# Optimization experiments

Hardware: AMD Instinct MI355X
Metric: run time of the kernel (lower is better)

Reference implementation:

```python
import jax, jax.numpy as jnp
import numpy as np

ALPHA = 2.0   # ATan surrogate alpha (spikingjelly default)
VTH = 0.5     # v_threshold
NUM_HEADS = 8

@jax.custom_vjp
def atan_spike(x):
    return (x >= 0.0).astype(x.dtype)

def _atan_fwd(x):
    return atan_spike(x), x

def _atan_bwd(x, g):
    return (g * (ALPHA / 2.0) / (1.0 + (jnp.pi / 2.0 * ALPHA * x) ** 2),)

atan_spike.defvjp(_atan_fwd, _atan_bwd)

def lif(x, w):
    # ParametricLIFNode, step_mode='m', decay_input=True, v_reset=0 (hard reset), detach_reset
    sg = jax.nn.sigmoid(w)
    def step(v, xt):
        v = v + (xt - v) * sg
        s = atan_spike(v - VTH)
        v = v * (1.0 - jax.lax.stop_gradient(s))  # hard reset to 0, detached
        return v, s
    _, spikes = jax.lax.scan(step, jnp.zeros_like(x[0]), x)
    return spikes

def bn_eT(x, gamma, beta, eps=1e-5):
    # x: [T, B, C, N]; per-(T,C) channel stats over (B, N)  == BatchNorm1d on [B, T*C, N] (train mode)
    T, B, C, N = x.shape
    mean = x.mean(axis=(1, 3), keepdims=True)
    var = jnp.mean((x - mean) ** 2, axis=(1, 3), keepdims=True)
    g = gamma.reshape(T, 1, C, 1)
    b = beta.reshape(T, 1, C, 1)
    return (x - mean) * jax.lax.rsqrt(var + eps) * g + b

def setup_inputs() -> dict:
    key = jax.random.key(0)
    ks = jax.random.split(key, 6)
    T, B, N, C = 16, 8, 196, 512
    return {
        "x": jax.random.normal(ks[0], (T, B, N, C), dtype=jnp.float32),
        "qkv_w": jax.random.normal(ks[1], (3 * C, C), dtype=jnp.float32) * 0.02,
        "qkv_b": jax.random.normal(ks[2], (3 * C,), dtype=jnp.float32) * 0.02,
        "bn1_g": jnp.ones((T * 3 * C,), dtype=jnp.float32),
        "bn1_b": jnp.zeros((T * 3 * C,), dtype=jnp.float32),
        "proj_w": jax.random.normal(ks[3], (C, C), dtype=jnp.float32) * 0.02,
        "proj_b": jax.random.normal(ks[4], (C,), dtype=jnp.float32) * 0.02,
        "bn2_g": jnp.ones((T * C,), dtype=jnp.float32),
        "bn2_b": jnp.zeros((T * C,), dtype=jnp.float32),
        "w_in": jnp.zeros((), dtype=jnp.float32),
        "w_q": jnp.zeros((), dtype=jnp.float32),
        "w_k": jnp.zeros((), dtype=jnp.float32),
        "w_v": jnp.zeros((), dtype=jnp.float32),
        "w_proj": jnp.zeros((), dtype=jnp.float32),
    }

def reference(x, qkv_w, qkv_b, bn1_g, bn1_b, proj_w, proj_b, bn2_g, bn2_b,
              w_in, w_q, w_k, w_v, w_proj):
    T, B, N, C = x.shape
    H = NUM_HEADS
    hd = C // H
    scale = hd ** -0.5

    x = lif(x, w_in)                                            # [T,B,N,C] spikes
    qkv = jnp.einsum('tbnc,oc->tbno', x, qkv_w) + qkv_b         # [T,B,N,3C]
    qkv = bn_eT(jnp.swapaxes(qkv, -2, -1), bn1_g, bn1_b)        # [T,B,3C,N]
    qkv = jnp.swapaxes(qkv, -2, -1).reshape(T, B, N, 3, H, hd)
    qkv = jnp.transpose(qkv, (3, 0, 1, 4, 2, 5))                # [3,T,B,H,N,hd]

    q_sk = lif(qkv[0], w_q)
    k_sk = lif(qkv[1], w_k)
    v_sk = lif(qkv[2], w_v)

    kv = jnp.einsum('tbhnd,tbhne->tbhde', k_sk, v_sk)           # k^T @ v : [T,B,H,hd,hd]
    out = jnp.einsum('tbhnd,tbhde->tbhne', q_sk, kv) * scale    # [T,B,H,N,hd]
    out = jnp.transpose(out, (0, 1, 3, 2, 4)).reshape(T, B, N, C)

    out = lif(out, w_proj)
    out = jnp.einsum('tbnc,oc->tbno', out, proj_w) + proj_b     # [T,B,N,C]
    out = bn_eT(jnp.swapaxes(out, -2, -1), bn2_g, bn2_b)        # [T,B,C,N]
    return jnp.swapaxes(out, -2, -1)                            # [T,B,N,C]
```

## Files before the change

kernel.cpp:

```cpp
#include <hip/hip_runtime.h>


#define TT 16
#define BB 8
#define NNQ 196
#define CC 512
#define HH 8
#define HD 64
#define O3 1536
#define BN (BB*NNQ)
#define PT (BN*CC)
#define WTOT ((O3+CC)*CC)
#define NRG 14

static constexpr float VTH = 0.5f;
typedef __attribute__((ext_vector_type(8))) short short8;
typedef __attribute__((ext_vector_type(4))) float f32x4;
typedef unsigned short u16;

__device__ __forceinline__ float sigm(float w){ return 1.f/(1.f+expf(-w)); }

__device__ __forceinline__ float lif_step(float x, float& v, float sg){
  float d  = __fsub_rn(x, v);
  float dd = __fmul_rn(d, sg);
  v = __fadd_rn(v, dd);
  float sp = (v >= VTH) ? 1.f : 0.f;
  v = __fmul_rn(v, __fsub_rn(1.f, sp));
  return sp;
}

__device__ __forceinline__ u16 bf16_rn(float x){
  unsigned u = __float_as_uint(x);
  unsigned r = u + 0x7FFF + ((u>>16)&1);
  return (u16)(r>>16);
}
__device__ __forceinline__ float bf16_to_f(u16 h){
  return __uint_as_float(((unsigned)h)<<16);
}

__global__ void k_wsplit(const float* __restrict__ qkv_w, const float* __restrict__ proj_w,
                         u16* __restrict__ whi, u16* __restrict__ wmid, u16* __restrict__ wlo){
  int i = blockIdx.x*256 + threadIdx.x;
  float w = (i < O3*CC) ? qkv_w[i] : proj_w[i - O3*CC];
  u16 h = bf16_rn(w);          float r1 = w - bf16_to_f(h);
  u16 m = bf16_rn(r1);         float r2 = r1 - bf16_to_f(m);
  u16 l = bf16_rn(r2);
  whi[i]=h; wmid[i]=m; wlo[i]=l;
}

__global__ void k_lif_x(const float* __restrict__ x, const float* __restrict__ w,
                        float* __restrict__ vin, u16* __restrict__ s0, int t0, int tc){
  int g = blockIdx.x*256 + threadIdx.x;
  float sg = sigm(w[0]);
  float v = (t0==0) ? 0.f : vin[g];
  for (int tt=0; tt<tc; ++tt){
    float sp = lif_step(x[(size_t)(t0+tt)*PT + g], v, sg);
    s0[(size_t)tt*PT + g] = (sp!=0.f) ? 0x3F80 : 0;
  }
  vin[g] = v;
}

template<int ON>
__global__ __launch_bounds__(256)
void k_gemm_mfma(const u16* __restrict__ A, const u16* __restrict__ Wh,
                 const u16* __restrict__ Wm, const u16* __restrict__ Wl,
                 const float* __restrict__ bias, float* __restrict__ Cm, int M){
  __shared__ __align__(16) u16 Al[128][64];
  __shared__ __align__(16) u16 Bh[128][64];
  __shared__ __align__(16) u16 Bm[128][64];
  __shared__ __align__(16) u16 Bl[128][64];
  int tid = threadIdx.x;
  int w = tid>>6, lane = tid&63;
  int m0 = blockIdx.x*128, o0 = blockIdx.y*128;
  int wm = (w&1)*64, wn = (w>>1)*64;
  int r16 = lane&15, kg = lane>>4;
  f32x4 acc[4][4] = {};
  for (int k0=0;k0<512;k0+=64){
    #pragma unroll
    for (int i=0;i<4;++i){
      int u = tid*4 + i;
      int row = u>>3, slot = u&7;
      int sl = slot ^ (row&7);
      int gr = m0+row; if (gr>=M) gr=M-1;
      *(float4*)&Al[row][sl*8] = *(const float4*)&A [(size_t)gr*512      + k0 + slot*8];
      *(float4*)&Bh[row][sl*8] = *(const float4*)&Wh[(size_t)(o0+row)*512 + k0 + slot*8];
      *(float4*)&Bm[row][sl*8] = *(const float4*)&Wm[(size_t)(o0+row)*512 + k0 + slot*8];
      *(float4*)&Bl[row][sl*8] = *(const float4*)&Wl[(size_t)(o0+row)*512 + k0 + slot*8];
    }
    __syncthreads();
    #pragma unroll
    for (int s=0;s<2;++s){
      short8 af[4], bh[4], bm[4], bl[4];
      #pragma unroll
      for (int mt=0;mt<4;++mt){
        int r = wm + mt*16 + r16;
        af[mt] = *(const short8*)&Al[r][((s*4+kg)^(r&7))*8];
      }
      #pragma unroll
      for (int nt=0;nt<4;++nt){
        int r = wn + nt*16 + r16;
        int sl = ((s*4+kg)^(r&7))*8;
        bh[nt] = *(const short8*)&Bh[r][sl];
        bm[nt] = *(const short8*)&Bm[r][sl];
        bl[nt] = *(const short8*)&Bl[r][sl];
      }
      #pragma unroll
      for (int mt=0;mt<4;++mt)
        #pragma unroll
        for (int nt=0;nt<4;++nt){
          acc[mt][nt] = __builtin_amdgcn_mfma_f32_16x16x32_bf16(af[mt], bh[nt], acc[mt][nt],0,0,0);
          acc[mt][nt] = __builtin_amdgcn_mfma_f32_16x16x32_bf16(af[mt], bm[nt], acc[mt][nt],0,0,0);
          acc[mt][nt] = __builtin_amdgcn_mfma_f32_16x16x32_bf16(af[mt], bl[nt], acc[mt][nt],0,0,0);
        }
    }
    __syncthreads();
  }
  #pragma unroll
  for (int mt=0; mt<4; ++mt)
    #pragma unroll
    for (int nt=0; nt<4; ++nt){
      int o = o0 + wn + nt*16 + r16;
      float bs = bias[o];
      #pragma unroll
      for (int i=0;i<4;++i){
        int m = m0 + wm + mt*16 + kg*4 + i;
        if (m < M) Cm[(size_t)m*ON + o] = acc[mt][nt][i] + bs;
      }
    }
}

template<int O>
__global__ void k_stat_part(const float* __restrict__ X, double* __restrict__ psum,
                            double* __restrict__ psq){
  int o = blockIdx.x*64 + threadIdx.x;
  int tt = blockIdx.y;
  int rg = blockIdx.z;
  const float* Xb = X + (size_t)tt*BN*O;
  int r0 = rg*112;
  double sum=0.0, sq=0.0;
  for (int i=r0+threadIdx.y; i<r0+112; i+=4){
    double v = (double)Xb[(size_t)i*O + o];
    sum += v; sq += v*v;
  }
  __shared__ double ssum[4][64], ssq[4][64];
  ssum[threadIdx.y][threadIdx.x]=sum;
  ssq [threadIdx.y][threadIdx.x]=sq;
  __syncthreads();
  if (threadIdx.y==0){
    double s = ssum[0][threadIdx.x]+ssum[1][threadIdx.x]+ssum[2][threadIdx.x]+ssum[3][threadIdx.x];
    double q = ssq [0][threadIdx.x]+ssq [1][threadIdx.x]+ssq [2][threadIdx.x]+ssq [3][threadIdx.x];
    size_t idx = ((size_t)tt*O + o)*NRG + rg;
    psum[idx]=s; psq[idx]=q;
  }
}

template<int O, int TCN>
__global__ void k_stat_reduce(const double* __restrict__ psum, const double* __restrict__ psq,
                              float* __restrict__ mean, float* __restrict__ rstd){
  int i = blockIdx.x*256 + threadIdx.x;
  if (i >= TCN*O) return;
  double s=0.0, q=0.0;
  #pragma unroll
  for (int g=0; g<NRG; ++g){ s += psum[(size_t)i*NRG+g]; q += psq[(size_t)i*NRG+g]; }
  double m = s*(1.0/BN);
  double var = q*(1.0/BN) - m*m;
  mean[i]=(float)m;
  rstd[i]=(float)(1.0/sqrt(var+1e-5));
}

__global__ void k_lif_qkv(const float* __restrict__ qkv, const float* __restrict__ mean,
                          const float* __restrict__ rstd, const float* __restrict__ g1,
                          const float* __restrict__ b1,
                          const float* __restrict__ wq, const float* __restrict__ wk,
                          const float* __restrict__ wv,
                          float* __restrict__ vq, float* __restrict__ vk, float* __restrict__ vv,
                          u16* __restrict__ qs, u16* __restrict__ ks,
                          u16* __restrict__ vs, int t0, int tc){
  int g = blockIdx.x*256 + threadIdx.x;
  int j = blockIdx.y;
  int d = g & 63;
  int n = (g>>6) % NNQ;
  int h = (g/(NNQ*64)) & 7;
  int b = g/(NNQ*64*8);
  int o = j*CC + h*HD + d;
  const float* w = (j==0)? wq : (j==1)? wk : wv;
  float* st  = (j==0)? vq : (j==1)? vk : vv;
  u16* out = (j==0)? qs : (j==1)? ks : vs;
  float sg = sigm(w[0]);
  float v = (t0==0) ? 0.f : st[g];
  size_t row = (size_t)(b*NNQ + n)*O3 + o;
  for (int tt=0; tt<tc; ++tt){
    float xv = qkv[(size_t)tt*BN*O3 + row];
    int so = tt*O3 + o;
    int go = (t0+tt)*O3 + o;
    float xn = __fadd_rn(__fmul_rn(__fmul_rn(__fsub_rn(xv, mean[so]), rstd[so]),
                                   g1[go]), b1[go]);
    float sp = lif_step(xn, v, sg);
    out[(size_t)tt*PT + g] = (sp!=0.f) ? 0x3F80 : 0;
  }
  st[g] = v;
}

__global__ __launch_bounds__(256)
void k_kvqv_mfma(const u16* __restrict__ ks, const u16* __restrict__ vs,
                 const u16* __restrict__ qs, float* __restrict__ attn){
  __shared__ __align__(16) u16 Kb[224][64];
  __shared__ __align__(16) u16 Vb[224][64];
  __shared__ __align__(16) u16 kvb[64][64];
  int blk = blockIdx.x;
  size_t base = (size_t)blk * (NNQ*HD);
  int tid = threadIdx.x, w = tid>>6, lane = tid&63;
  int r16 = lane&15, kg = lane>>4;
  for (int u=tid; u<224*8; u+=256){
    int row=u>>3, slot=u&7;
    float4 z = {0.f,0.f,0.f,0.f};
    float4 kd = z, vd = z;
    if (row < NNQ){
      kd = *(const float4*)&ks[base + (size_t)row*64 + slot*8];
      vd = *(const float4*)&vs[base + (size_t)row*64 + slot*8];
    }
    *(float4*)&Kb[row][slot*8] = kd;
    *(float4*)&Vb[row][slot*8] = vd;
  }
  __syncthreads();
  f32x4 acc[4] = {};
  int d0 = w*16;
  for (int n0=0;n0<224;n0+=32){
    short8 af;
    #pragma unroll
    for (int jj=0;jj<8;++jj) af[jj] = (short)Kb[n0+kg*8+jj][d0 + r16];
    #pragma unroll
    for (int nt=0;nt<4;++nt){
      short8 bf;
      #pragma unroll
      for (int jj=0;jj<8;++jj) bf[jj] = (short)Vb[n0+kg*8+jj][nt*16 + r16];
      acc[nt] = __builtin_amdgcn_mfma_f32_16x16x32_bf16(af, bf, acc[nt],0,0,0);
    }
  }
  #pragma unroll
  for (int nt=0;nt<4;++nt)
    #pragma unroll
    for (int i=0;i<4;++i)
      kvb[d0 + kg*4 + i][nt*16 + r16] = (u16)(__float_as_uint(acc[nt][i])>>16);
  __syncthreads();
  for (int u=tid; u<224*8; u+=256){
    int row=u>>3, slot=u&7;
    int sl = slot ^ (row&7);
    float4 qd = {0.f,0.f,0.f,0.f};
    if (row < NNQ) qd = *(const float4*)&qs[base + (size_t)row*64 + slot*8];
    *(float4*)&Kb[row][sl*8] = qd;
  }
  __syncthreads();
  short8 bkv[2][4];
  #pragma unroll
  for (int s=0;s<2;++s)
    #pragma unroll
    for (int nt=0;nt<4;++nt){
      short8 bf;
      #pragma unroll
      for (int jj=0;jj<8;++jj) bf[jj] = (short)kvb[s*32 + kg*8 + jj][nt*16 + r16];
      bkv[s][nt] = bf;
    }
  for (int mt=w; mt<13; mt+=4){
    f32x4 a2[4] = {};
    short8 qa[2];
    #pragma unroll
    for (int s=0;s<2;++s){
      int r = mt*16 + r16;
      qa[s] = *(const short8*)&Kb[r][(((s*4+kg)^(r&7)))*8];
    }
    #pragma unroll
    for (int s=0;s<2;++s)
      #pragma unroll
      for (int nt=0;nt<4;++nt)
        a2[nt] = __builtin_amdgcn_mfma_f32_16x16x32_bf16(qa[s], bkv[s][nt], a2[nt],0,0,0);
    #pragma unroll
    for (int nt=0;nt<4;++nt){
      int e = nt*16 + r16;
      #pragma unroll
      for (int i=0;i<4;++i){
        int n = mt*16 + kg*4 + i;
        if (n < NNQ) attn[base + (size_t)n*64 + e] = a2[nt][i]*0.125f;
      }
    }
  }
}

__global__ void k_lif_attn(const float* __restrict__ ain, const float* __restrict__ w,
                           float* __restrict__ vo, u16* __restrict__ sp, int t0, int tc){
  int g = blockIdx.x*256 + threadIdx.x;
  int e = g & 63;
  int n = (g>>6) % NNQ;
  int h = (g/(NNQ*64)) & 7;
  int b = g/(NNQ*64*8);
  size_t dst = (size_t)(b*NNQ + n)*CC + h*HD + e;
  float sg = sigm(w[0]);
  float v = (t0==0) ? 0.f : vo[g];
  for (int tt=0; tt<tc; ++tt){
    float s = lif_step(ain[(size_t)tt*PT + g], v, sg);
    sp[(size_t)tt*PT + dst] = (s!=0.f) ? 0x3F80 : 0;
  }
  vo[g] = v;
}

__global__ void k_bn2_apply(const float* __restrict__ X, const float* __restrict__ mean,
                            const float* __restrict__ rstd, const float* __restrict__ g2,
                            const float* __restrict__ b2, float* __restrict__ Y, int t0){
  size_t idx = ((size_t)blockIdx.x*256 + threadIdx.x)*4;
  int tt = (int)(idx / PT);
  size_t off = idx - (size_t)tt*PT;
  int c = (int)(off & (CC-1));
  float4 xv = *(const float4*)&X[idx];
  float4 mv = *(const float4*)&mean[tt*CC + c];
  float4 rv = *(const float4*)&rstd[tt*CC + c];
  float4 gv = *(const float4*)&g2[(t0+tt)*CC + c];
  float4 bv = *(const float4*)&b2[(t0+tt)*CC + c];
  float4 yv;
  yv.x = __fadd_rn(__fmul_rn(__fmul_rn(__fsub_rn(xv.x, mv.x), rv.x), gv.x), bv.x);
  yv.y = __fadd_rn(__fmul_rn(__fmul_rn(__fsub_rn(xv.y, mv.y), rv.y), gv.y), bv.y);
  yv.z = __fadd_rn(__fmul_rn(__fmul_rn(__fsub_rn(xv.z, mv.z), rv.z), gv.z), bv.z);
  yv.w = __fadd_rn(__fmul_rn(__fmul_rn(__fsub_rn(xv.w, mv.w), rv.w), gv.w), bv.w);
  *(float4*)&Y[(size_t)(t0+tt)*PT + off] = yv;
}

extern "C" void kernel_launch(void* const* d_in, const int* in_sizes, int n_in,
                              void* d_out, int out_size, void* d_ws, size_t ws_size,
                              hipStream_t stream){
  const float* x      = (const float*)d_in[0];
  const float* qkv_w  = (const float*)d_in[1];
  const float* qkv_b  = (const float*)d_in[2];
  const float* bn1_g  = (const float*)d_in[3];
  const float* bn1_b  = (const float*)d_in[4];
  const float* proj_w = (const float*)d_in[5];
  const float* proj_b = (const float*)d_in[6];
  const float* bn2_g  = (const float*)d_in[7];
  const float* bn2_b  = (const float*)d_in[8];
  const float* w_in   = (const float*)d_in[9];
  const float* w_q    = (const float*)d_in[10];
  const float* w_k    = (const float*)d_in[11];
  const float* w_v    = (const float*)d_in[12];
  const float* w_proj = (const float*)d_in[13];
  float* outp = (float*)d_out;

  auto need = [](int tc)->size_t{
    return 4ull*5*PT + 8ull*tc*O3 + 8ull*tc*CC
         + 16ull*tc*O3*NRG + 16ull*tc*CC*NRG
         + 6ull*WTOT
         + 10ull*tc*PT
         + 4ull*tc*BN*O3;
  };
  int TC = 16;
  while (TC > 1 && need(TC) > ws_size) TC >>= 1;

  char* p = (char*)d_ws;
  float* vin = (float*)p; p += 4ull*PT;
  float* vq  = (float*)p; p += 4ull*PT;
  float* vk  = (float*)p; p += 4ull*PT;
  float* vv  = (float*)p; p += 4ull*PT;
  float* vo  = (float*)p; p += 4ull*PT;
  float* mean1 = (float*)p; p += 4ull*TC*O3;
  float* rstd1 = (float*)p; p += 4ull*TC*O3;
  float* mean2 = (float*)p; p += 4ull*TC*CC;
  float* rstd2 = (float*)p; p += 4ull*TC*CC;
  double* p1sum = (double*)p; p += 8ull*TC*O3*NRG;
  double* p1sq  = (double*)p; p += 8ull*TC*O3*NRG;
  double* p2sum = (double*)p; p += 8ull*TC*CC*NRG;
  double* p2sq  = (double*)p; p += 8ull*TC*CC*NRG;
  u16* whi  = (u16*)p; p += 2ull*WTOT;
  u16* wmid = (u16*)p; p += 2ull*WTOT;
  u16* wlo  = (u16*)p; p += 2ull*WTOT;
  u16* s0    = (u16*)p; p += 2ull*TC*PT;
  u16* qsb   = (u16*)p; p += 2ull*TC*PT;
  u16* ksb   = (u16*)p; p += 2ull*TC*PT;
  u16* vsb   = (u16*)p; p += 2ull*TC*PT;
  u16* sproj = (u16*)p; p += 2ull*TC*PT;
  float* qkv_all = (float*)p;
  float* attn    = qkv_all;
  float* projo   = qkv_all + (size_t)TC*PT;

  k_wsplit<<<WTOT/256, 256, 0, stream>>>(qkv_w, proj_w, whi, wmid, wlo);

  for (int t0=0; t0<TT; t0+=TC){
    int M = TC*BN;
    k_lif_x<<<PT/256, 256, 0, stream>>>(x, w_in, vin, s0, t0, TC);

    k_gemm_mfma<O3><<<dim3((M+127)/128, O3/128), 256, 0, stream>>>(
        s0, whi, wmid, wlo, qkv_b, qkv_all, M);

    k_stat_part<O3><<<dim3(O3/64, TC, NRG), dim3(64,4), 0, stream>>>(qkv_all, p1sum, p1sq);
    if (TC == 16)
      k_stat_reduce<O3,16><<<(16*O3+255)/256, 256, 0, stream>>>(p1sum, p1sq, mean1, rstd1);
    else if (TC == 8)
      k_stat_reduce<O3,8><<<(8*O3+255)/256, 256, 0, stream>>>(p1sum, p1sq, mean1, rstd1);
    else
      k_stat_reduce<O3,4><<<(4*O3+255)/256, 256, 0, stream>>>(p1sum, p1sq, mean1, rstd1);

    k_lif_qkv<<<dim3(PT/256, 3), 256, 0, stream>>>(qkv_all, mean1, rstd1, bn1_g, bn1_b,
                                                   w_q, w_k, w_v, vq, vk, vv,
                                                   qsb, ksb, vsb, t0, TC);

    k_kvqv_mfma<<<TC*BB*HH, 256, 0, stream>>>(ksb, vsb, qsb, attn);

    k_lif_attn<<<PT/256, 256, 0, stream>>>(attn, w_proj, vo, sproj, t0, TC);

    k_gemm_mfma<CC><<<dim3((M+127)/128, CC/128), 256, 0, stream>>>(
        sproj, whi + (size_t)O3*CC, wmid + (size_t)O3*CC, wlo + (size_t)O3*CC,
        proj_b, projo, M);

    k_stat_part<CC><<<dim3(CC/64, TC, NRG), dim3(64,4), 0, stream>>>(projo, p2sum, p2sq);
    if (TC == 16)
      k_stat_reduce<CC,16><<<(16*CC+255)/256, 256, 0, stream>>>(p2sum, p2sq, mean2, rstd2);
    else if (TC == 8)
      k_stat_reduce<CC,8><<<(8*CC+255)/256, 256, 0, stream>>>(p2sum, p2sq, mean2, rstd2);
    else
      k_stat_reduce<CC,4><<<(4*CC+255)/256, 256, 0, stream>>>(p2sum, p2sq, mean2, rstd2);

    k_bn2_apply<<<(TC*(size_t)PT)/1024, 256, 0, stream>>>(projo, mean2, rstd2,
                                                          bn2_g, bn2_b, outp, t0);
  }
}
```

Measured before the change: 465.8 us.

## Use direct global-to-LDS loads and XCD-aware tile remapping in the MFMA GEMM

Replaces the register-staged float4 global→LDS copies in the bf16x3 GEMM with the global_load_lds builtin, which writes straight into shared memory. The XOR swizzle is now applied on the global source column so each wave writes contiguous LDS rows. The 2D grid becomes a 1D grid whose block IDs are remapped so consecutive tiles land on the same XCD, aiming for better L2 reuse of the A rows and weight tiles. There is still no double buffering, and the swizzle now depends on the wave-uniform LDS destination layout lining up with lane order.

Measured after the change: 410.9 us. -11.8%, faster.

```diff
diff --git a/kernel.cpp b/kernel.cpp
--- a/kernel.cpp
+++ b/kernel.cpp
@@ -38,6 +38,12 @@
   return __uint_as_float(((unsigned)h)<<16);
 }
 
+__device__ __forceinline__ void gld_lds16(const void* g, void* l){
+  __builtin_amdgcn_global_load_lds(
+    (const __attribute__((address_space(1))) unsigned int*)g,
+    (__attribute__((address_space(3))) unsigned int*)l, 16, 0, 0);
+}
+
 __global__ void k_wsplit(const float* __restrict__ qkv_w, const float* __restrict__ proj_w,
                          u16* __restrict__ whi, u16* __restrict__ wmid, u16* __restrict__ wlo){
   int i = blockIdx.x*256 + threadIdx.x;
@@ -69,23 +75,32 @@
   __shared__ __align__(16) u16 Bh[128][64];
   __shared__ __align__(16) u16 Bm[128][64];
   __shared__ __align__(16) u16 Bl[128][64];
+  const int nON = ON/128;
+  int nwg = gridDim.x;
+  int bid = blockIdx.x;
+  int q = nwg >> 3, r = nwg & 7;
+  int xcd = bid & 7, idx = bid >> 3;
+  int wgid = (xcd < r ? xcd*(q+1) : r*(q+1) + (xcd-r)*q) + idx;
+  int mb = wgid / nON, ob = wgid - mb*nON;
+  int m0 = mb*128, o0 = ob*128;
+
   int tid = threadIdx.x;
   int w = tid>>6, lane = tid&63;
-  int m0 = blockIdx.x*128, o0 = blockIdx.y*128;
   int wm = (w&1)*64, wn = (w>>1)*64;
   int r16 = lane&15, kg = lane>>4;
+  int lrow = w*32 + (lane>>3);
+  int lslot = lane&7;
   f32x4 acc[4][4] = {};
   for (int k0=0;k0<512;k0+=64){
     #pragma unroll
     for (int i=0;i<4;++i){
-      int u = tid*4 + i;
-      int row = u>>3, slot = u&7;
-      int sl = slot ^ (row&7);
+      int row = lrow + i*8;
+      int gslot = lslot ^ (row&7);
       int gr = m0+row; if (gr>=M) gr=M-1;
-      *(float4*)&Al[row][sl*8] = *(const float4*)&A [(size_t)gr*512      + k0 + slot*8];
-      *(float4*)&Bh[row][sl*8] = *(const float4*)&Wh[(size_t)(o0+row)*512 + k0 + slot*8];
-      *(float4*)&Bm[row][sl*8] = *(const float4*)&Wm[(size_t)(o0+row)*512 + k0 + slot*8];
-      *(float4*)&Bl[row][sl*8] = *(const float4*)&Wl[(size_t)(o0+row)*512 + k0 + slot*8];
+      gld_lds16(&A [(size_t)gr*512       + k0 + gslot*8], &Al[w*32+i*8][0]);
+      gld_lds16(&Wh[(size_t)(o0+row)*512 + k0 + gslot*8], &Bh[w*32+i*8][0]);
+      gld_lds16(&Wm[(size_t)(o0+row)*512 + k0 + gslot*8], &Bm[w*32+i*8][0]);
+      gld_lds16(&Wl[(size_t)(o0+row)*512 + k0 + gslot*8], &Bl[w*32+i*8][0]);
     }
     __syncthreads();
     #pragma unroll
@@ -93,16 +108,16 @@
       short8 af[4], bh[4], bm[4], bl[4];
       #pragma unroll
       for (int mt=0;mt<4;++mt){
-        int r = wm + mt*16 + r16;
-        af[mt] = *(const short8*)&Al[r][((s*4+kg)^(r&7))*8];
+        int rr = wm + mt*16 + r16;
+        af[mt] = *(const short8*)&Al[rr][((s*4+kg)^(rr&7))*8];
       }
       #pragma unroll
       for (int nt=0;nt<4;++nt){
-        int r = wn + nt*16 + r16;
-        int sl = ((s*4+kg)^(r&7))*8;
-        bh[nt] = *(const short8*)&Bh[r][sl];
-        bm[nt] = *(const short8*)&Bm[r][sl];
-        bl[nt] = *(const short8*)&Bl[r][sl];
+        int rr = wn + nt*16 + r16;
+        int sl = ((s*4+kg)^(rr&7))*8;
+        bh[nt] = *(const short8*)&Bh[rr][sl];
+        bm[nt] = *(const short8*)&Bm[rr][sl];
+        bl[nt] = *(const short8*)&Bl[rr][sl];
       }
       #pragma unroll
       for (int mt=0;mt<4;++mt)
@@ -266,8 +281,8 @@
     short8 qa[2];
     #pragma unroll
     for (int s=0;s<2;++s){
-      int r = mt*16 + r16;
-      qa[s] = *(const short8*)&Kb[r][(((s*4+kg)^(r&7)))*8];
+      int rr = mt*16 + r16;
+      qa[s] = *(const short8*)&Kb[rr][(((s*4+kg)^(rr&7)))*8];
     }
     #pragma unroll
     for (int s=0;s<2;++s)
@@ -382,9 +397,10 @@
 
   for (int t0=0; t0<TT; t0+=TC){
     int M = TC*BN;
+    int nMB = (M+127)/128;
     k_lif_x<<<PT/256, 256, 0, stream>>>(x, w_in, vin, s0, t0, TC);
 
-    k_gemm_mfma<O3><<<dim3((M+127)/128, O3/128), 256, 0, stream>>>(
+    k_gemm_mfma<O3><<<nMB*(O3/128), 256, 0, stream>>>(
         s0, whi, wmid, wlo, qkv_b, qkv_all, M);
 
     k_stat_part<O3><<<dim3(O3/64, TC, NRG), dim3(64,4), 0, stream>>>(qkv_all, p1sum, p1sq);
@@ -403,7 +419,7 @@
 
     k_lif_attn<<<PT/256, 256, 0, stream>>>(attn, w_proj, vo, sproj, t0, TC);
 
-    k_gemm_mfma<CC><<<dim3((M+127)/128, CC/128), 256, 0, stream>>>(
+    k_gemm_mfma<CC><<<nMB*(CC/128), 256, 0, stream>>>(
         sproj, whi + (size_t)O3*CC, wmid + (size_t)O3*CC, wlo + (size_t)O3*CC,
         proj_b, projo, M);
 
```
